# Kernel optimization log

Measured on AMD Instinct MI355X. Metric: run time of the kernel, lower is better.

Reference implementation:

```python
import jax, jax.numpy as jnp
import numpy as np

EPS = 1e-5

def _ln(x, g, b):
    m = jnp.mean(x, axis=-1, keepdims=True)
    v = jnp.var(x, axis=-1, keepdims=True)
    return (x - m) / jnp.sqrt(v + EPS) * g + b

def _partition(x, nw):
    b, h, w, c = x.shape
    x = x.reshape(b, nw, h // nw, nw, w // nw, c).transpose(0, 1, 3, 2, 4, 5)
    return x.reshape(b * nw * nw, h // nw, w // nw, c)

def _merge(x, nw):
    b_, h, w, c = x.shape
    b = b_ // (nw * nw)
    x = x.reshape(b, nw, nw, h, w, c).transpose(0, 1, 3, 2, 4, 5)
    return x.reshape(b, nw * h, nw * w, c)

def _window_attn(q, k, v, width, height, nw, mask):
    b, _, c = q.shape
    q = q.reshape(b, height, width, c)
    k = k.reshape(b, height, width, c)
    v = v.reshape(b, height, width, c)
    sh, sw = (height // nw) // 2, (width // nw) // 2
    q = jnp.roll(q, (-sh, -sw), (1, 2))
    k = jnp.roll(k, (-sh, -sw), (1, 2))
    v = jnp.roll(v, (-sh, -sw), (1, 2))
    q = _partition(q, nw); k = _partition(k, nw); v = _partition(v, nw)
    N = (height // nw) * (width // nw)
    b_ = b * nw * nw
    qf = q.reshape(b_, N, c); kf = k.reshape(b_, N, c); vf = v.reshape(b_, N, c)
    scale = jnp.asarray(c, qf.dtype) ** 0.5
    scores = jnp.einsum('bnc,bmc->bnm', qf, kf) / scale  # [b_, N, N]
    scores = (scores.reshape(b, nw * nw, N, N) + mask[None]).reshape(b_, N, N)
    attn = jax.nn.softmax(scores, axis=-1)
    out = jnp.einsum('bnm,bmc->bnc', attn, vf)
    out = _merge(out.reshape(b_, height // nw, width // nw, c), nw)
    out = jnp.roll(out, (sh, sw), (1, 2))
    return out.reshape(b, height * width, c)

def _block(feat0, feat1, width, height, mask, nw, wq, wk, wv, wfc, g, be, ffn=None):
    q = feat0 @ wq; k = feat1 @ wk; v = feat1 @ wv
    a = _window_attn(q, k, v, width, height, nw, mask)
    a = _ln(a @ wfc, g, be)
    if ffn is not None:
        w1, w2, fg, fb = ffn
        h = jax.nn.gelu(jnp.concatenate([feat0, a], axis=-1) @ w1, approximate=False)
        a = _ln(h @ w2, fg, fb)
    return feat0 + a

def setup_inputs() -> dict:
    key = jax.random.key(0)
    B, H, W, NW, D = 8, 128, 128, 8, 256
    N = (H // NW) * (W // NW)
    ks = jax.random.split(key, 16)
    s = D ** -0.5
    return {
        'feat0': jax.random.normal(ks[0], (B, H * W, D), jnp.float32),
        'feat1': jax.random.normal(ks[1], (B, H * W, D), jnp.float32),
        'mask_attn': jax.random.normal(ks[2], (NW * NW, N, N), jnp.float32),
        'width': W, 'height': H, 'n_window': NW,
        'intra_wq': jax.random.normal(ks[3], (D, D), jnp.float32) * s,
        'intra_wk': jax.random.normal(ks[4], (D, D), jnp.float32) * s,
        'intra_wv': jax.random.normal(ks[5], (D, D), jnp.float32) * s,
        'intra_wfc': jax.random.normal(ks[6], (D, D), jnp.float32) * s,
        'intra_g': jnp.ones((D,), jnp.float32),
        'intra_b': jnp.zeros((D,), jnp.float32),
        'inter_wq': jax.random.normal(ks[7], (D, D), jnp.float32) * s,
        'inter_wk': jax.random.normal(ks[8], (D, D), jnp.float32) * s,
        'inter_wv': jax.random.normal(ks[9], (D, D), jnp.float32) * s,
        'inter_wfc': jax.random.normal(ks[10], (D, D), jnp.float32) * s,
        'inter_g': jnp.ones((D,), jnp.float32),
        'inter_b': jnp.zeros((D,), jnp.float32),
        'inter_w1': jax.random.normal(ks[11], (2 * D, 2 * D * 4), jnp.float32) * (2 * D) ** -0.5,
        'inter_w2': jax.random.normal(ks[12], (2 * D * 4, D), jnp.float32) * (2 * D * 4) ** -0.5,
        'inter_fg': jnp.ones((D,), jnp.float32),
        'inter_fb': jnp.zeros((D,), jnp.float32),
    }

def reference(feat0, feat1, mask_attn, width, height, n_window,
              intra_wq, intra_wk, intra_wv, intra_wfc, intra_g, intra_b,
              inter_wq, inter_wk, inter_wv, inter_wfc, inter_g, inter_b,
              inter_w1, inter_w2, inter_fg, inter_fb):
    f0 = _block(feat0, feat0, width, height, mask_attn, n_window,
                intra_wq, intra_wk, intra_wv, intra_wfc, intra_g, intra_b)
    out = _block(f0, feat1, width, height, mask_attn, n_window,
                 inter_wq, inter_wk, inter_wv, inter_wfc, inter_g, inter_b,
                 ffn=(inter_w1, inter_w2, inter_fg, inter_fb))
    return out
```

## Files before the change

### kernel.cpp

```cpp
#include <hip/hip_runtime.h>

typedef unsigned short u16;
typedef unsigned int   u32;

using f32x4  = __attribute__((ext_vector_type(4))) float;
using bf16x8 = __attribute__((ext_vector_type(8))) __bf16;

__device__ inline u16 f2bf(float f) {
  return __builtin_bit_cast(u16, (__bf16)f);
}
__device__ inline float bf2f(u16 v) {
  u32 u = ((u32)v) << 16;
  return __builtin_bit_cast(float, u);
}

__device__ inline void gl_lds16(const u16* g, u16* l) {
  __builtin_amdgcn_global_load_lds((const __attribute__((address_space(1))) void*)g,
                                   (__attribute__((address_space(3))) void*)l,
                                   16, 0, 0);
}

__device__ inline int perm_fwd(int m) {
  int b = m >> 14, rem = m & 16383;
  int h = rem >> 7, w = rem & 127;
  int hr = (h - 8) & 127, wr = (w - 8) & 127;
  int win = (b << 6) | ((hr >> 4) << 3) | (wr >> 4);
  return (win << 8) | ((hr & 15) << 4) | (wr & 15);
}
__device__ inline int perm_inv(int r) {
  int win = r >> 8, t = r & 255;
  int b = win >> 6, wy = (win >> 3) & 7, wx = win & 7;
  int h = (((wy << 4) | (t >> 4)) + 8) & 127;
  int w = (((wx << 4) | (t & 15)) + 8) & 127;
  return (b << 14) | (h << 7) | w;
}


enum { MODE_QKV = 0, MODE_SCORES = 1, MODE_PV = 2, MODE_F32 = 3, MODE_FFN1 = 4 };

template<int MODE>
__global__ __launch_bounds__(256)
void gemm_nt(const u16* __restrict__ A, int lda, long long sAz,
             const u16* __restrict__ Bt, int ldb, long long sBz,
             u16* __restrict__ OutB, float* __restrict__ OutF,
             const float* __restrict__ mask, int K, int ldo)
{
  __shared__ __align__(16) u16 sA[128 * 64];
  __shared__ __align__(16) u16 sB[128 * 64];

  const int tid  = threadIdx.x;
  const int lane = tid & 63;
  const int wave = tid >> 6;
  const int l15  = lane & 15;
  const int quad = lane >> 4;
  const int wm   = (wave >> 1) << 6;
  const int wn   = (wave & 1) << 6;
  const int z    = blockIdx.z;
  const int m0   = (int)(blockIdx.y) << 7;
  const int n0   = (int)(blockIdx.x) << 7;

  const u16* Ab = A  + (long long)z * sAz;
  const u16* Bb = Bt + (long long)z * sBz;

  const int cd = ((lane & 7) ^ ((lane >> 3) & 7)) << 3;
  const int rs = (wave << 5) + (lane >> 3);
  const u16* ga0 = Ab + (long long)(m0 + rs) * lda + cd;
  const u16* gb0 = Bb + (long long)(n0 + rs) * ldb + cd;
  u16* la0 = &sA[wave << 11];
  u16* lb0 = &sB[wave << 11];

  const f32x4 zero = {0.f, 0.f, 0.f, 0.f};
  f32x4 acc[4][4];
#pragma unroll
  for (int i = 0; i < 4; ++i)
#pragma unroll
    for (int j = 0; j < 4; ++j) acc[i][j] = zero;

  for (int k0 = 0; k0 < K; k0 += 64) {
    __syncthreads();
#pragma unroll
    for (int p = 0; p < 4; ++p) {
      gl_lds16(ga0 + k0 + (p << 3) * lda, la0 + (p << 9));
      gl_lds16(gb0 + k0 + (p << 3) * ldb, lb0 + (p << 9));
    }
    __syncthreads();
#pragma unroll
    for (int kk = 0; kk < 2; ++kk) {
      const int sw = (((quad | (kk << 2)) ^ (l15 & 7)) << 3);
      bf16x8 af[4], bfr[4];
#pragma unroll
      for (int i = 0; i < 4; ++i) {
        af[i]  = *(const bf16x8*)(sA + ((wm + (i << 4) + l15) << 6) + sw);
        bfr[i] = *(const bf16x8*)(sB + ((wn + (i << 4) + l15) << 6) + sw);
      }
#pragma unroll
      for (int i = 0; i < 4; ++i)
#pragma unroll
        for (int j = 0; j < 4; ++j)
          acc[i][j] = __builtin_amdgcn_mfma_f32_16x16x32_bf16(af[i], bfr[j], acc[i][j], 0, 0, 0);
    }
  }

#pragma unroll
  for (int i = 0; i < 4; ++i) {
#pragma unroll
    for (int r = 0; r < 4; ++r) {
      int mg = m0 + wm + (i << 4) + (quad << 2) + r;
      if constexpr (MODE == MODE_QKV) {
        u16* orow = OutB + ((long long)perm_fwd(mg) << 8);
#pragma unroll
        for (int j = 0; j < 4; ++j) {
          int ng = n0 + wn + (j << 4) + l15;
          orow[ng] = f2bf(acc[i][j][r]);
        }
      } else if constexpr (MODE == MODE_PV) {
        u16* orow = OutB + ((long long)perm_inv((z << 8) + mg) << 8);
#pragma unroll
        for (int j = 0; j < 4; ++j) {
          int ng = n0 + wn + (j << 4) + l15;
          orow[ng] = f2bf(acc[i][j][r]);
        }
      } else if constexpr (MODE == MODE_F32) {
        float* orow = OutF + ((long long)mg << 8);
#pragma unroll
        for (int j = 0; j < 4; ++j) {
          int ng = n0 + wn + (j << 4) + l15;
          orow[ng] = acc[i][j][r];
        }
      } else {
        u16* orow = OutB + (long long)mg * ldo;
#pragma unroll
        for (int j = 0; j < 4; ++j) {
          int ng = n0 + wn + (j << 4) + l15;
          float v = acc[i][j][r];
          float t = v * fmaf(v * v, -0.071354816f, -1.5957691216f);
          float g = v * __builtin_amdgcn_rcpf(1.0f + __expf(t));
          orow[ng] = f2bf(g);
        }
      }
    }
  }
}

__global__ __launch_bounds__(256)
void scores_softmax(const u16* __restrict__ Q, const u16* __restrict__ Kw,
                    const float* __restrict__ mask, u16* __restrict__ SP)
{
  __shared__ __align__(16) u16 sA[128 * 64];
  __shared__ __align__(16) u16 sB[256 * 64];

  const int tid  = threadIdx.x;
  const int lane = tid & 63;
  const int wave = tid >> 6;
  const int l15  = lane & 15;
  const int quad = lane >> 4;

  const int mhalf = (int)blockIdx.x;
  const int z     = (int)blockIdx.y;
  const int m0    = mhalf << 7;

  const u16* Ab = Q  + ((long long)z << 16);
  const u16* Bb = Kw + ((long long)z << 16);

  const int cd  = ((lane & 7) ^ ((lane >> 3) & 7)) << 3;
  const int rsA = (wave << 5) + (lane >> 3);
  const int rsB = (wave << 6) + (lane >> 3);
  const u16* ga0 = Ab + (long long)(m0 + rsA) * 256 + cd;
  const u16* gb0 = Bb + (long long)rsB * 256 + cd;
  u16* la0 = &sA[wave << 11];
  u16* lb0 = &sB[wave << 12];

  const f32x4 zero = {0.f, 0.f, 0.f, 0.f};
  f32x4 acc[2][16];
#pragma unroll
  for (int i = 0; i < 2; ++i)
#pragma unroll
    for (int j = 0; j < 16; ++j) acc[i][j] = zero;

  for (int k0 = 0; k0 < 256; k0 += 64) {
    __syncthreads();
#pragma unroll
    for (int p = 0; p < 4; ++p)
      gl_lds16(ga0 + k0 + (p << 3) * 256, la0 + (p << 9));
#pragma unroll
    for (int p = 0; p < 8; ++p)
      gl_lds16(gb0 + k0 + (p << 3) * 256, lb0 + (p << 9));
    __syncthreads();
#pragma unroll
    for (int kk = 0; kk < 2; ++kk) {
      const int sw = (((quad | (kk << 2)) ^ (l15 & 7)) << 3);
      bf16x8 af0 = *(const bf16x8*)(sA + (((wave << 5) + l15) << 6) + sw);
      bf16x8 af1 = *(const bf16x8*)(sA + (((wave << 5) + 16 + l15) << 6) + sw);
#pragma unroll
      for (int j = 0; j < 16; ++j) {
        bf16x8 bf = *(const bf16x8*)(sB + (((j << 4) + l15) << 6) + sw);
        acc[0][j] = __builtin_amdgcn_mfma_f32_16x16x32_bf16(af0, bf, acc[0][j], 0, 0, 0);
        acc[1][j] = __builtin_amdgcn_mfma_f32_16x16x32_bf16(af1, bf, acc[1][j], 0, 0, 0);
      }
    }
  }

  const float* mbase = mask + (((long long)(z & 63)) << 16);
#pragma unroll
  for (int i = 0; i < 2; ++i) {
#pragma unroll
    for (int r = 0; r < 4; ++r) {
      const int mg = m0 + (wave << 5) + (i << 4) + (quad << 2) + r;
      const float* mrow = mbase + ((long long)mg << 8);
      float sv[16];
      float mx = -3.0e38f;
#pragma unroll
      for (int j = 0; j < 16; ++j) {
        sv[j] = acc[i][j][r] * 0.0625f + mrow[(j << 4) + l15];
        mx = fmaxf(mx, sv[j]);
      }
#pragma unroll
      for (int o = 1; o < 16; o <<= 1) mx = fmaxf(mx, __shfl_xor(mx, o));
      float sum = 0.f;
#pragma unroll
      for (int j = 0; j < 16; ++j) { sv[j] = __expf(sv[j] - mx); sum += sv[j]; }
#pragma unroll
      for (int o = 1; o < 16; o <<= 1) sum += __shfl_xor(sum, o);
      const float inv = 1.0f / sum;
      u16* orow = SP + (((long long)z) << 16) + ((long long)mg << 8);
#pragma unroll
      for (int j = 0; j < 16; ++j) orow[(j << 4) + l15] = f2bf(sv[j] * inv);
    }
  }
}

enum { LN_XCAT0 = 0, LN_XCAT1 = 1, LN_OUT = 2 };

template<int MODE>
__global__ __launch_bounds__(256)
void gemm_ln(const u16* __restrict__ A, int lda,
             const u16* __restrict__ Bt,
             const float* __restrict__ G, const float* __restrict__ Bias,
             const float* __restrict__ ResF, const u16* __restrict__ ResB,
             float* __restrict__ OutF, u16* __restrict__ OutB, int K)
{
  __shared__ __align__(16) u16 sA[64 * 64];
  __shared__ __align__(16) u16 sB[256 * 64];

  const int tid  = threadIdx.x;
  const int lane = tid & 63;
  const int wave = tid >> 6;
  const int l15  = lane & 15;
  const int quad = lane >> 4;
  const int m0   = (int)blockIdx.x << 6;

  const int cd  = ((lane & 7) ^ ((lane >> 3) & 7)) << 3;
  const int rsA = (wave << 4) + (lane >> 3);
  const int rsB = (wave << 6) + (lane >> 3);
  const u16* ga0 = A  + (long long)(m0 + rsA) * lda + cd;
  const u16* gb0 = Bt + (long long)rsB * K + cd;
  u16* la0 = &sA[wave << 10];
  u16* lb0 = &sB[wave << 12];

  const f32x4 zero = {0.f, 0.f, 0.f, 0.f};
  f32x4 acc[16];
#pragma unroll
  for (int j = 0; j < 16; ++j) acc[j] = zero;

  for (int k0 = 0; k0 < K; k0 += 64) {
    __syncthreads();
#pragma unroll
    for (int p = 0; p < 2; ++p)
      gl_lds16(ga0 + k0 + (p << 3) * lda, la0 + (p << 9));
#pragma unroll
    for (int p = 0; p < 8; ++p)
      gl_lds16(gb0 + k0 + (p << 3) * K, lb0 + (p << 9));
    __syncthreads();
#pragma unroll
    for (int kk = 0; kk < 2; ++kk) {
      const int sw = (((quad | (kk << 2)) ^ (l15 & 7)) << 3);
      bf16x8 af = *(const bf16x8*)(sA + (((wave << 4) + l15) << 6) + sw);
#pragma unroll
      for (int j = 0; j < 16; ++j) {
        bf16x8 bf = *(const bf16x8*)(sB + (((j << 4) + l15) << 6) + sw);
        acc[j] = __builtin_amdgcn_mfma_f32_16x16x32_bf16(af, bf, acc[j], 0, 0, 0);
      }
    }
  }

  float gj[16], bj[16];
#pragma unroll
  for (int j = 0; j < 16; ++j) {
    gj[j] = G[(j << 4) + l15];
    bj[j] = Bias[(j << 4) + l15];
  }

#pragma unroll
  for (int r = 0; r < 4; ++r) {
    const int mg = m0 + (wave << 4) + (quad << 2) + r;
    float s = 0.f, s2 = 0.f;
#pragma unroll
    for (int j = 0; j < 16; ++j) {
      float v = acc[j][r];
      s += v; s2 += v * v;
    }
#pragma unroll
    for (int o = 1; o < 16; o <<= 1) { s += __shfl_xor(s, o); s2 += __shfl_xor(s2, o); }
    const float mean = s * (1.0f / 256.0f);
    const float var  = s2 * (1.0f / 256.0f) - mean * mean;
    const float rstd = rsqrtf(var + 1e-5f);
    if constexpr (MODE == LN_XCAT0) {
      u16* orow = OutB + ((long long)mg << 9);
      const float* rrow = ResF + ((long long)mg << 8);
#pragma unroll
      for (int j = 0; j < 16; ++j) {
        float v = (acc[j][r] - mean) * rstd * gj[j] + bj[j];
        orow[(j << 4) + l15] = f2bf(v + rrow[(j << 4) + l15]);
      }
    } else if constexpr (MODE == LN_XCAT1) {
      u16* orow = OutB + ((long long)mg << 9) + 256;
#pragma unroll
      for (int j = 0; j < 16; ++j) {
        float v = (acc[j][r] - mean) * rstd * gj[j] + bj[j];
        orow[(j << 4) + l15] = f2bf(v);
      }
    } else {
      const u16* rrow = ResB + ((long long)mg << 9);
      float* orow = OutF + ((long long)mg << 8);
#pragma unroll
      for (int j = 0; j < 16; ++j) {
        float v = (acc[j][r] - mean) * rstd * gj[j] + bj[j];
        orow[(j << 4) + l15] = v + bf2f(rrow[(j << 4) + l15]);
      }
    }
  }
}

__global__ __launch_bounds__(256)
void transpose256(const u16* __restrict__ src, u16* __restrict__ dst)
{
  __shared__ u16 t[32][33];
  const int z  = blockIdx.z;
  const int tx = blockIdx.x << 5;
  const int ty = blockIdx.y << 5;
  const int c  = threadIdx.x & 31;
  const int r0 = threadIdx.x >> 5;
  const long long base = ((long long)z) << 16;
#pragma unroll
  for (int p = 0; p < 4; ++p) {
    int r = r0 + (p << 3);
    t[r][c] = src[base + (long long)(ty + r) * 256 + tx + c];
  }
  __syncthreads();
#pragma unroll
  for (int p = 0; p < 4; ++p) {
    int r = r0 + (p << 3);
    dst[base + (long long)(tx + r) * 256 + ty + c] = t[c][r];
  }
}

__global__ __launch_bounds__(256)
void cvt_f32_bf16(const float* __restrict__ src, u16* __restrict__ dst, int n4)
{
  int i = blockIdx.x * 256 + threadIdx.x;
  if (i >= n4) return;
  float4 v = ((const float4*)src)[i];
  ushort4 u; u.x = f2bf(v.x); u.y = f2bf(v.y); u.z = f2bf(v.z); u.w = f2bf(v.w);
  ((ushort4*)dst)[i] = u;
}

__global__ __launch_bounds__(256)
void wtrans(const float* __restrict__ src, u16* __restrict__ dst, int R, int C)
{
  int idx = blockIdx.x * 256 + threadIdx.x;
  if (idx >= R * C) return;
  int r = idx / C, c = idx - r * C;
  dst[c * R + r] = f2bf(src[idx]);
}

extern "C" void kernel_launch(void* const* d_in, const int* in_sizes, int n_in,
                              void* d_out, int out_size, void* d_ws, size_t ws_size,
                              hipStream_t stream)
{
  (void)in_sizes; (void)n_in; (void)out_size;
  const float* feat0 = (const float*)d_in[0];
  const float* feat1 = (const float*)d_in[1];
  const float* mask  = (const float*)d_in[2];
  const float* wq1 = (const float*)d_in[6];
  const float* wk1 = (const float*)d_in[7];
  const float* wv1 = (const float*)d_in[8];
  const float* wf1 = (const float*)d_in[9];
  const float* g1  = (const float*)d_in[10];
  const float* b1  = (const float*)d_in[11];
  const float* wq2 = (const float*)d_in[12];
  const float* wk2 = (const float*)d_in[13];
  const float* wv2 = (const float*)d_in[14];
  const float* wf2 = (const float*)d_in[15];
  const float* g2  = (const float*)d_in[16];
  const float* b2  = (const float*)d_in[17];
  const float* w1  = (const float*)d_in[18];
  const float* w2  = (const float*)d_in[19];
  const float* fg  = (const float*)d_in[20];
  const float* fb  = (const float*)d_in[21];

  const size_t Mi = 1048576;
  const size_t WB = 4 * Mi;
  const int Mtot = 131072;

  int nc = 8;
  for (int c = 1; c <= 8; c <<= 1) {
    size_t S = (size_t)(Mtot / c) * 512;
    if (7 * S + WB <= ws_size) { nc = c; break; }
  }
  const int Mc = Mtot / nc;
  const size_t S = (size_t)Mc * 512;

  char* ws = (char*)d_ws;
  u16*   featb = (u16*)(ws);
  u16*   SPb   = featb;
  u16*   qw    = (u16*)(ws + S);
  u16*   Ob    = qw;
  u16*   hbuf  = featb;
  u16*   kw    = (u16*)(ws + 2 * S);
  u16*   vw    = (u16*)(ws + 3 * S);
  u16*   vt    = (u16*)(ws + 4 * S);
  u16*   xcat  = (u16*)(ws + 5 * S);
  u16*   wb    = (u16*)(ws + 7 * S);
  u16* wq1t = wb;            u16* wk1t = wb + 65536;  u16* wv1t = wb + 131072; u16* wf1t = wb + 196608;
  u16* wq2t = wb + 262144;   u16* wk2t = wb + 327680; u16* wv2t = wb + 393216; u16* wf2t = wb + 458752;
  u16* w1t  = wb + 524288;
  u16* w2t  = wb + 524288 + 1048576;

  const dim3 blk(256);
  const dim3 gBig(2, Mc / 128, 1);
  const int  Wc = Mc / 256;
  const dim3 gWin(2, 2, Wc);
  const dim3 gSS(2, Wc);
  const dim3 gTr(8, 8, Wc);
  const int  gRows = Mc / 4;
  const int  gLN   = Mc / 64;
  const int  MF = Mc / 4;
  const dim3 gF1(16, MF / 128, 1);
  const int  gLNF  = MF / 64;

  wtrans<<<256, blk, 0, stream>>>(wq1, wq1t, 256, 256);
  wtrans<<<256, blk, 0, stream>>>(wk1, wk1t, 256, 256);
  wtrans<<<256, blk, 0, stream>>>(wv1, wv1t, 256, 256);
  wtrans<<<256, blk, 0, stream>>>(wf1, wf1t, 256, 256);
  wtrans<<<256, blk, 0, stream>>>(wq2, wq2t, 256, 256);
  wtrans<<<256, blk, 0, stream>>>(wk2, wk2t, 256, 256);
  wtrans<<<256, blk, 0, stream>>>(wv2, wv2t, 256, 256);
  wtrans<<<256, blk, 0, stream>>>(wf2, wf2t, 256, 256);
  wtrans<<<4096, blk, 0, stream>>>(w1, w1t, 512, 2048);
  wtrans<<<2048, blk, 0, stream>>>(w2, w2t, 2048, 256);

  for (int c = 0; c < nc; ++c) {
    const long long off = (long long)c * Mc * 256;
    const float* f0in = feat0 + off;
    const float* f1in = feat1 + off;
    float* outp = (float*)d_out + off;

    cvt_f32_bf16<<<gRows, blk, 0, stream>>>(f0in, featb, Mc * 64);
    gemm_nt<MODE_QKV><<<gBig, blk, 0, stream>>>(featb, 256, 0, wq1t, 256, 0, qw, nullptr, nullptr, 256, 0);
    gemm_nt<MODE_QKV><<<gBig, blk, 0, stream>>>(featb, 256, 0, wk1t, 256, 0, kw, nullptr, nullptr, 256, 0);
    gemm_nt<MODE_QKV><<<gBig, blk, 0, stream>>>(featb, 256, 0, wv1t, 256, 0, vw, nullptr, nullptr, 256, 0);
    transpose256<<<gTr, blk, 0, stream>>>(vw, vt);
    scores_softmax<<<gSS, blk, 0, stream>>>(qw, kw, mask, SPb);
    gemm_nt<MODE_PV><<<gWin, blk, 0, stream>>>(SPb, 256, 65536, vt, 256, 65536, Ob, nullptr, nullptr, 256, 0);
    gemm_ln<LN_XCAT0><<<gLN, blk, 0, stream>>>(Ob, 256, wf1t, g1, b1, f0in, nullptr, nullptr, xcat, 256);

    cvt_f32_bf16<<<gRows, blk, 0, stream>>>(f1in, featb, Mc * 64);
    gemm_nt<MODE_QKV><<<gBig, blk, 0, stream>>>(xcat, 512, 0, wq2t, 256, 0, qw, nullptr, nullptr, 256, 0);
    gemm_nt<MODE_QKV><<<gBig, blk, 0, stream>>>(featb, 256, 0, wk2t, 256, 0, kw, nullptr, nullptr, 256, 0);
    gemm_nt<MODE_QKV><<<gBig, blk, 0, stream>>>(featb, 256, 0, wv2t, 256, 0, vw, nullptr, nullptr, 256, 0);
    transpose256<<<gTr, blk, 0, stream>>>(vw, vt);
    scores_softmax<<<gSS, blk, 0, stream>>>(qw, kw, mask, SPb);
    gemm_nt<MODE_PV><<<gWin, blk, 0, stream>>>(SPb, 256, 65536, vt, 256, 65536, Ob, nullptr, nullptr, 256, 0);
    gemm_ln<LN_XCAT1><<<gLN, blk, 0, stream>>>(Ob, 256, wf2t, g2, b2, nullptr, nullptr, nullptr, xcat, 256);

    for (int mc = 0; mc < 4; ++mc) {
      const u16* xc = xcat + (long long)mc * MF * 512;
      gemm_nt<MODE_FFN1><<<gF1, blk, 0, stream>>>(xc, 512, 0, w1t, 512, 0,
                                                  hbuf, nullptr, nullptr, 512, 2048);
      gemm_ln<LN_OUT><<<gLNF, blk, 0, stream>>>(hbuf, 2048, w2t, fg, fb, nullptr,
                                                xcat + (long long)mc * MF * 512,
                                                outp + (long long)mc * MF * 256, nullptr, 2048);
    }
  }
}
```

Baseline: 1.680 ms.

## Fuse Q/K projections, compute V directly transposed, enlarge FFN chunks

```diff
diff --git a/kernel.cpp b/kernel.cpp
--- a/kernel.cpp
+++ b/kernel.cpp
@@ -36,7 +36,7 @@
 }
 
 
-enum { MODE_QKV = 0, MODE_SCORES = 1, MODE_PV = 2, MODE_F32 = 3, MODE_FFN1 = 4 };
+enum { MODE_QKV = 0, MODE_PV = 2, MODE_FFN1 = 4 };
 
 template<int MODE>
 __global__ __launch_bounds__(256)
@@ -107,25 +107,18 @@
     for (int r = 0; r < 4; ++r) {
       int mg = m0 + wm + (i << 4) + (quad << 2) + r;
       if constexpr (MODE == MODE_QKV) {
-        u16* orow = OutB + ((long long)perm_fwd(mg) << 8);
+        u16* orow = OutB + (long long)(n0 >> 8) * ldo + ((long long)perm_fwd(mg) << 8);
+#pragma unroll
+        for (int j = 0; j < 4; ++j) {
+          int ng = n0 + wn + (j << 4) + l15;
+          orow[ng & 255] = f2bf(acc[i][j][r]);
+        }
+      } else if constexpr (MODE == MODE_PV) {
+        u16* orow = OutB + ((long long)perm_inv((z << 8) + mg) << 8);
 #pragma unroll
         for (int j = 0; j < 4; ++j) {
           int ng = n0 + wn + (j << 4) + l15;
           orow[ng] = f2bf(acc[i][j][r]);
-        }
-      } else if constexpr (MODE == MODE_PV) {
-        u16* orow = OutB + ((long long)perm_inv((z << 8) + mg) << 8);
-#pragma unroll
-        for (int j = 0; j < 4; ++j) {
-          int ng = n0 + wn + (j << 4) + l15;
-          orow[ng] = f2bf(acc[i][j][r]);
-        }
-      } else if constexpr (MODE == MODE_F32) {
-        float* orow = OutF + ((long long)mg << 8);
-#pragma unroll
-        for (int j = 0; j < 4; ++j) {
-          int ng = n0 + wn + (j << 4) + l15;
-          orow[ng] = acc[i][j][r];
         }
       } else {
         u16* orow = OutB + (long long)mg * ldo;
@@ -143,6 +136,84 @@
 }
 
 __global__ __launch_bounds__(256)
+void gemm_vt(const u16* __restrict__ Wt,
+             const u16* __restrict__ Feat,
+             u16* __restrict__ Vt)
+{
+  __shared__ __align__(16) u16 sA[128 * 64];
+  __shared__ __align__(16) u16 sB[128 * 64];
+
+  const int tid  = threadIdx.x;
+  const int lane = tid & 63;
+  const int wave = tid >> 6;
+  const int l15  = lane & 15;
+  const int quad = lane >> 4;
+  const int wm   = (wave >> 1) << 6;
+  const int wn   = (wave & 1) << 6;
+  const int z    = blockIdx.z;
+  const int m0   = (int)(blockIdx.y) << 7;
+  const int n0   = (int)(blockIdx.x) << 7;
+
+  const int cd = ((lane & 7) ^ ((lane >> 3) & 7)) << 3;
+  const int rs = (wave << 5) + (lane >> 3);
+  const u16* ga0 = Wt + (long long)(m0 + rs) * 256 + cd;
+  const u16* gb0 = Feat + (long long)perm_inv((z << 8) + n0 + rs)        * 256 + cd;
+  const u16* gb1 = Feat + (long long)perm_inv((z << 8) + n0 + rs + 8)    * 256 + cd;
+  const u16* gb2 = Feat + (long long)perm_inv((z << 8) + n0 + rs + 16)   * 256 + cd;
+  const u16* gb3 = Feat + (long long)perm_inv((z << 8) + n0 + rs + 24)   * 256 + cd;
+  u16* la0 = &sA[wave << 11];
+  u16* lb0 = &sB[wave << 11];
+
+  const f32x4 zero = {0.f, 0.f, 0.f, 0.f};
+  f32x4 acc[4][4];
+#pragma unroll
+  for (int i = 0; i < 4; ++i)
+#pragma unroll
+    for (int j = 0; j < 4; ++j) acc[i][j] = zero;
+
+  for (int k0 = 0; k0 < 256; k0 += 64) {
+    __syncthreads();
+#pragma unroll
+    for (int p = 0; p < 4; ++p)
+      gl_lds16(ga0 + k0 + (p << 3) * 256, la0 + (p << 9));
+    gl_lds16(gb0 + k0, lb0);
+    gl_lds16(gb1 + k0, lb0 + 512);
+    gl_lds16(gb2 + k0, lb0 + 1024);
+    gl_lds16(gb3 + k0, lb0 + 1536);
+    __syncthreads();
+#pragma unroll
+    for (int kk = 0; kk < 2; ++kk) {
+      const int sw = (((quad | (kk << 2)) ^ (l15 & 7)) << 3);
+      bf16x8 af[4], bfr[4];
+#pragma unroll
+      for (int i = 0; i < 4; ++i) {
+        af[i]  = *(const bf16x8*)(sA + ((wm + (i << 4) + l15) << 6) + sw);
+        bfr[i] = *(const bf16x8*)(sB + ((wn + (i << 4) + l15) << 6) + sw);
+      }
+#pragma unroll
+      for (int i = 0; i < 4; ++i)
+#pragma unroll
+        for (int j = 0; j < 4; ++j)
+          acc[i][j] = __builtin_amdgcn_mfma_f32_16x16x32_bf16(af[i], bfr[j], acc[i][j], 0, 0, 0);
+    }
+  }
+
+#pragma unroll
+  for (int i = 0; i < 4; ++i) {
+#pragma unroll
+    for (int r = 0; r < 4; ++r) {
+      const int mg = m0 + wm + (i << 4) + (quad << 2) + r;
+      u16* orow = Vt + (((long long)z) << 16) + ((long long)mg << 8);
+#pragma unroll
+      for (int j = 0; j < 4; ++j) {
+        int ng = n0 + wn + (j << 4) + l15;
+        orow[ng] = f2bf(acc[i][j][r]);
+      }
+    }
+  }
+}
+
+__global__ __launch_bounds__(256)
 void scores_softmax(const u16* __restrict__ Q, const u16* __restrict__ Kw,
                     const float* __restrict__ mask, u16* __restrict__ SP)
 {
@@ -328,29 +399,6 @@
         orow[(j << 4) + l15] = v + bf2f(rrow[(j << 4) + l15]);
       }
     }
-  }
-}
-
-__global__ __launch_bounds__(256)
-void transpose256(const u16* __restrict__ src, u16* __restrict__ dst)
-{
-  __shared__ u16 t[32][33];
-  const int z  = blockIdx.z;
-  const int tx = blockIdx.x << 5;
-  const int ty = blockIdx.y << 5;
-  const int c  = threadIdx.x & 31;
-  const int r0 = threadIdx.x >> 5;
-  const long long base = ((long long)z) << 16;
-#pragma unroll
-  for (int p = 0; p < 4; ++p) {
-    int r = r0 + (p << 3);
-    t[r][c] = src[base + (long long)(ty + r) * 256 + tx + c];
-  }
-  __syncthreads();
-#pragma unroll
-  for (int p = 0; p < 4; ++p) {
-    int r = r0 + (p << 3);
-    dst[base + (long long)(tx + r) * 256 + ty + c] = t[c][r];
   }
 }
 
@@ -417,7 +465,6 @@
   u16*   Ob    = qw;
   u16*   hbuf  = featb;
   u16*   kw    = (u16*)(ws + 2 * S);
-  u16*   vw    = (u16*)(ws + 3 * S);
   u16*   vt    = (u16*)(ws + 4 * S);
   u16*   xcat  = (u16*)(ws + 5 * S);
   u16*   wb    = (u16*)(ws + 7 * S);
@@ -428,13 +475,13 @@
 
   const dim3 blk(256);
   const dim3 gBig(2, Mc / 128, 1);
+  const dim3 gQK(4, Mc / 128, 1);
   const int  Wc = Mc / 256;
   const dim3 gWin(2, 2, Wc);
   const dim3 gSS(2, Wc);
-  const dim3 gTr(8, 8, Wc);
   const int  gRows = Mc / 4;
   const int  gLN   = Mc / 64;
-  const int  MF = Mc / 4;
+  const int  MF = Mc / 2;
   const dim3 gF1(16, MF / 128, 1);
   const int  gLNF  = MF / 64;
 
@@ -449,6 +496,8 @@
   wtrans<<<4096, blk, 0, stream>>>(w1, w1t, 512, 2048);
   wtrans<<<2048, blk, 0, stream>>>(w2, w2t, 2048, 256);
 
+  const int qkStride = Mc * 256;
+
   for (int c = 0; c < nc; ++c) {
     const long long off = (long long)c * Mc * 256;
     const float* f0in = feat0 + off;
@@ -456,24 +505,21 @@
     float* outp = (float*)d_out + off;
 
     cvt_f32_bf16<<<gRows, blk, 0, stream>>>(f0in, featb, Mc * 64);
-    gemm_nt<MODE_QKV><<<gBig, blk, 0, stream>>>(featb, 256, 0, wq1t, 256, 0, qw, nullptr, nullptr, 256, 0);
-    gemm_nt<MODE_QKV><<<gBig, blk, 0, stream>>>(featb, 256, 0, wk1t, 256, 0, kw, nullptr, nullptr, 256, 0);
-    gemm_nt<MODE_QKV><<<gBig, blk, 0, stream>>>(featb, 256, 0, wv1t, 256, 0, vw, nullptr, nullptr, 256, 0);
-    transpose256<<<gTr, blk, 0, stream>>>(vw, vt);
+    gemm_nt<MODE_QKV><<<gQK, blk, 0, stream>>>(featb, 256, 0, wq1t, 256, 0, qw, nullptr, nullptr, 256, qkStride);
+    gemm_vt<<<gWin, blk, 0, stream>>>(wv1t, featb, vt);
     scores_softmax<<<gSS, blk, 0, stream>>>(qw, kw, mask, SPb);
     gemm_nt<MODE_PV><<<gWin, blk, 0, stream>>>(SPb, 256, 65536, vt, 256, 65536, Ob, nullptr, nullptr, 256, 0);
     gemm_ln<LN_XCAT0><<<gLN, blk, 0, stream>>>(Ob, 256, wf1t, g1, b1, f0in, nullptr, nullptr, xcat, 256);
 
     cvt_f32_bf16<<<gRows, blk, 0, stream>>>(f1in, featb, Mc * 64);
-    gemm_nt<MODE_QKV><<<gBig, blk, 0, stream>>>(xcat, 512, 0, wq2t, 256, 0, qw, nullptr, nullptr, 256, 0);
+    gemm_nt<MODE_QKV><<<gBig, blk, 0, stream>>>(xcat, 512, 0, wq2t, 256, 0, qw, nullptr, nullptr, 512, 0);
     gemm_nt<MODE_QKV><<<gBig, blk, 0, stream>>>(featb, 256, 0, wk2t, 256, 0, kw, nullptr, nullptr, 256, 0);
-    gemm_nt<MODE_QKV><<<gBig, blk, 0, stream>>>(featb, 256, 0, wv2t, 256, 0, vw, nullptr, nullptr, 256, 0);
-    transpose256<<<gTr, blk, 0, stream>>>(vw, vt);
+    gemm_vt<<<gWin, blk, 0, stream>>>(wv2t, featb, vt);
     scores_softmax<<<gSS, blk, 0, stream>>>(qw, kw, mask, SPb);
     gemm_nt<MODE_PV><<<gWin, blk, 0, stream>>>(SPb, 256, 65536, vt, 256, 65536, Ob, nullptr, nullptr, 256, 0);
     gemm_ln<LN_XCAT1><<<gLN, blk, 0, stream>>>(Ob, 256, wf2t, g2, b2, nullptr, nullptr, nullptr, xcat, 256);
 
-    for (int mc = 0; mc < 4; ++mc) {
+    for (int mc = 0; mc < 2; ++mc) {
       const u16* xc = xcat + (long long)mc * MF * 512;
       gemm_nt<MODE_FFN1><<<gF1, blk, 0, stream>>>(xc, 512, 0, w1t, 512, 0,
                                                   hbuf, nullptr, nullptr, 512, 2048);
```

Result: faster. 1.633 ms (-2.8%).
